# Kernel tuning notes

Hardware: AMD Instinct MI355X
Metric: run time of the kernel (lower is better)

## Reference

```python
import jax, jax.numpy as jnp
import numpy as np


def setup_inputs() -> dict:
    key = jax.random.key(0)
    k1, k2 = jax.random.split(key)
    d, T, n = 256, 8192, 64
    # scale down so exp(ht^T D^T D hj) stays in range, as typical trained D would
    H = jax.random.normal(k1, (d, T), dtype=jnp.float32) * 0.1
    D = jax.random.normal(k2, (n, d), dtype=jnp.float32) * 0.1
    l2 = jnp.ones((), dtype=jnp.float32)
    return {"H": H, "D": D, "l2": l2}


def reference(H, D, l2):
    # H: [d, T], D: [n, d]
    DH = D @ H                                   # [n, T] = D @ H_T.T
    # S[t, j] = h_t^T (D^T D) h_j  == (DH)^T (DH)
    S = jnp.einsum('nt,nj->tj', DH, DH)          # [T, T]
    # beta_j = exp(-0.5 * ||D h_j||^2); row t: attn[t,:] = beta * exp(S[t,:]) / sum
    log_beta = -0.5 * jnp.sum(DH * DH, axis=0)   # [T]
    attn_map = jax.nn.softmax(S + log_beta[None, :], axis=1)  # [T, T]
    Z = l2 * (H @ attn_map)                      # [d, T]
    return Z
```

## Files before the change

kernel.cpp:

```cpp
#include <hip/hip_runtime.h>

#define T_DIM 8192
#define D_DIM 256
#define N_DIM 64
#define LOG2E 1.44269504f

typedef __bf16 bf16x8 __attribute__((ext_vector_type(8)));
typedef __bf16 bf16x4 __attribute__((ext_vector_type(4)));
typedef float f32x16 __attribute__((ext_vector_type(16)));

__device__ __forceinline__ f32x16 zero16() {
  f32x16 v;
#pragma unroll
  for (int i = 0; i < 16; ++i) v[i] = 0.f;
  return v;
}


__global__ __launch_bounds__(256) void k_dh(const float* __restrict__ H,
                                            const float* __restrict__ Dm,
                                            __bf16* __restrict__ DHf,
                                            float* __restrict__ lbe,
                                            float* __restrict__ rowsum) {
  __shared__ __bf16 HlThi[64 * 264];
  __shared__ __bf16 HlTlo[64 * 264];
  __shared__ __bf16 DHs[64 * 72];
  const int tid = threadIdx.x;
  const int t0 = blockIdx.x * 64;
  const int lane = tid & 63;
  const int wave = tid >> 6;
  const int h = lane >> 5;
  const int l31 = lane & 31;
  const float4* H4 = (const float4*)H;
#pragma unroll
  for (int r = 0; r < 16; ++r) {
    int idx = r * 256 + tid;
    int d = idx >> 4, tc = idx & 15;
    float4 v = H4[(size_t)d * (T_DIM / 4) + (t0 >> 2) + tc];
    float vv[4] = {v.x, v.y, v.z, v.w};
#pragma unroll
    for (int i = 0; i < 4; ++i) {
      __bf16 hi = (__bf16)vv[i];
      float lo = vv[i] - (float)hi;
      HlThi[(tc * 4 + i) * 264 + d] = hi;
      HlTlo[(tc * 4 + i) * 264 + d] = (__bf16)lo;
    }
  }
  __syncthreads();
  const int tt = wave & 1, nh = wave >> 1;
  const int m = tt * 32 + l31;
  const int n = nh * 32 + l31;
  f32x16 c = zero16();
  for (int kk = 0; kk < 16; ++kk) {
    bf16x8 ahi = *(const bf16x8*)&HlThi[m * 264 + kk * 16 + h * 8];
    bf16x8 alo = *(const bf16x8*)&HlTlo[m * 264 + kk * 16 + h * 8];
    const float4* dp = (const float4*)(Dm + (size_t)n * 256 + kk * 16 + h * 8);
    float4 b0 = dp[0], b1 = dp[1];
    float bv[8] = {b0.x, b0.y, b0.z, b0.w, b1.x, b1.y, b1.z, b1.w};
    bf16x8 bhi, blo;
#pragma unroll
    for (int i = 0; i < 8; ++i) {
      __bf16 hi = (__bf16)bv[i];
      bhi[i] = hi;
      blo[i] = (__bf16)(bv[i] - (float)hi);
    }
    c = __builtin_amdgcn_mfma_f32_32x32x16_bf16(ahi, bhi, c, 0, 0, 0);
    c = __builtin_amdgcn_mfma_f32_32x32x16_bf16(ahi, blo, c, 0, 0, 0);
    c = __builtin_amdgcn_mfma_f32_32x32x16_bf16(alo, bhi, c, 0, 0, 0);
  }
#pragma unroll
  for (int r = 0; r < 16; ++r) {
    int row = tt * 32 + (r & 3) + 8 * (r >> 2) + 4 * h;
    DHs[row * 72 + n] = (__bf16)c[r];
  }
  __syncthreads();
#pragma unroll
  for (int r = 0; r < 2; ++r) {
    int idx = r * 256 + tid;
    int g = idx >> 8, cc = (idx >> 5) & 7, l = idx & 31;
    bf16x8 w = *(const bf16x8*)&DHs[(g * 32 + l) * 72 + cc * 8];
    *(bf16x8*)(DHf + (size_t)(blockIdx.x * 2 + g) * 2048 + cc * 256 + l * 8) = w;
  }
  if (tid < 64) {
    float s = 0.f;
#pragma unroll
    for (int q = 0; q < 8; ++q) {
      bf16x8 w = *(const bf16x8*)&DHs[tid * 72 + q * 8];
#pragma unroll
      for (int i = 0; i < 8; ++i) { float f = (float)w[i]; s += f * f; }
    }
    lbe[t0 + tid] = -0.5f * s * LOG2E;
    rowsum[t0 + tid] = 0.f;
  }
}

__global__ __launch_bounds__(256, 2) void k_rowsum(const __bf16* __restrict__ DHf,
                                                   const float* __restrict__ lbe,
                                                   float* __restrict__ rowsum) {
  __shared__ float red2[64 * 65];
  const int tid = threadIdx.x;
  const int lane = tid & 63;
  const int wave = tid >> 6;
  const int h = lane >> 5;
  const int tt = wave & 1, jt = wave >> 1;
  const int t0 = (int)(blockIdx.x >> 4) * 64;
  const int jbase = (int)(blockIdx.x & 15) * 512;
  const int Gt = (t0 >> 5) + tt;
  bf16x8 aR[4];
#pragma unroll
  for (int kk = 0; kk < 4; ++kk)
    aR[kk] = *(const bf16x8*)(DHf + (size_t)Gt * 2048 + kk * 512 + lane * 8);
  float racc[16];
#pragma unroll
  for (int r = 0; r < 16; ++r) racc[r] = 0.f;
  for (int jit = 0; jit < 8; ++jit) {
    const size_t Gj = (jbase >> 5) + jit * 2 + jt;
    bf16x8 b[4];
#pragma unroll
    for (int kk = 0; kk < 4; ++kk)
      b[kk] = *(const bf16x8*)(DHf + Gj * 2048 + kk * 512 + lane * 8);
    const float lbv = lbe[jbase + jit * 64 + jt * 32 + (lane & 31)];
    f32x16 s = zero16();
#pragma unroll
    for (int kk = 0; kk < 4; ++kk)
      s = __builtin_amdgcn_mfma_f32_32x32x16_bf16(aR[kk], b[kk], s, 0, 0, 0);
#pragma unroll
    for (int r = 0; r < 16; ++r)
      racc[r] += __builtin_amdgcn_exp2f(__builtin_fmaf(s[r], LOG2E, lbv));
  }
#pragma unroll
  for (int r = 0; r < 16; ++r) {
    int tl = tt * 32 + (r & 3) + 8 * (r >> 2) + 4 * h;
    red2[tl * 65 + jt * 32 + (lane & 31)] = racc[r];
  }
  __syncthreads();
  if (tid < 64) {
    float s = 0.f;
#pragma unroll 8
    for (int c = 0; c < 64; ++c) s += red2[tid * 65 + c];
    atomicAdd(&rowsum[t0 + tid], s);
  }
}

__global__ __launch_bounds__(256) void k_scaleH(const float* __restrict__ H,
                                                const float* __restrict__ rowsum,
                                                __bf16* __restrict__ Hbf_sw,
                                                float* __restrict__ Z) {
  __shared__ float rinvL[64];
  const int tid = threadIdx.x;
  const int bx = blockIdx.x;
  const int tblk = bx >> 1, dh = bx & 1;
  const int t0 = tblk * 64;
  if (tid < 64) rinvL[tid] = 1.0f / rowsum[t0 + tid];
  __syncthreads();
#pragma unroll
  for (int itr = 0; itr < 4; ++itr) {
    int idx = itr * 256 + tid;
    int dl = idx >> 3, tbp = idx & 7;
    int d = dh * 128 + dl;
    int swz = (d ^ (d >> 3)) & 7;
    int tloc = (tbp ^ swz) << 3;
    const float4* hp = (const float4*)(H + (size_t)d * T_DIM + t0 + tloc);
    float4 v0 = hp[0], v1 = hp[1];
    float4 r0 = *(const float4*)&rinvL[tloc];
    float4 r1 = *(const float4*)&rinvL[tloc + 4];
    bf16x8 w;
    w[0] = (__bf16)(v0.x * r0.x); w[1] = (__bf16)(v0.y * r0.y);
    w[2] = (__bf16)(v0.z * r0.z); w[3] = (__bf16)(v0.w * r0.w);
    w[4] = (__bf16)(v1.x * r1.x); w[5] = (__bf16)(v1.y * r1.y);
    w[6] = (__bf16)(v1.z * r1.z); w[7] = (__bf16)(v1.w * r1.w);
    *(bf16x8*)(Hbf_sw + (size_t)tblk * 16384 + (size_t)d * 64 + tbp * 8) = w;
  }
  float4* Z4 = (float4*)Z;
  const int base = bx * 256 + tid;
  const float4 z4 = {0.f, 0.f, 0.f, 0.f};
#pragma unroll
  for (int r = 0; r < 8; ++r) Z4[r * 65536 + base] = z4;
}

__global__ __launch_bounds__(256, 2) void k_z(const __bf16* __restrict__ Hbf_sw,
                                              const __bf16* __restrict__ DHf,
                                              const float* __restrict__ lbe,
                                              const float* __restrict__ l2p,
                                              float* __restrict__ Z) {
  __shared__ __bf16 Hs[256 * 64];
  __shared__ __bf16 Pt[128 * 64];
  const int tid = threadIdx.x;
  const int lane = tid & 63;
  const int wave = tid >> 6;
  const int h = lane >> 5;
  const int l31 = lane & 31;
  const int bx = blockIdx.x;
  const int ts = bx & 7;
  const int j0 = (bx >> 3) * 128;
  const int tbase = ts * 1024;
  const float l2v = l2p[0];
  const int s_tt = wave & 1, s_jg = wave >> 1;
  bf16x8 bS[2][4];
  float lbv[2];
#pragma unroll
  for (int q = 0; q < 2; ++q) {
    const size_t Gj = (j0 >> 5) + s_jg * 2 + q;
#pragma unroll
    for (int kk = 0; kk < 4; ++kk)
      bS[q][kk] = *(const bf16x8*)(DHf + Gj * 2048 + kk * 512 + lane * 8);
    lbv[q] = lbe[j0 + (s_jg * 2 + q) * 32 + l31];
  }
  f32x16 acc[4][2];
#pragma unroll
  for (int u = 0; u < 4; ++u)
#pragma unroll
    for (int v = 0; v < 2; ++v) acc[u][v] = zero16();
  bf16x8 aR[4];
  {
    const size_t Gt = ts * 32 + s_tt;
#pragma unroll
    for (int kk = 0; kk < 4; ++kk)
      aR[kk] = *(const bf16x8*)(DHf + Gt * 2048 + kk * 512 + lane * 8);
  }
  for (int it = 0; it < 16; ++it) {
    const __bf16* gsrc = Hbf_sw + (size_t)(ts * 16 + it) * 16384;
#pragma unroll
    for (int r = 0; r < 8; ++r) {
      int chunk = wave * 8 + r;
      __builtin_amdgcn_global_load_lds(
          (const __attribute__((address_space(1))) unsigned int*)(gsrc + chunk * 512 + lane * 8),
          (__attribute__((address_space(3))) unsigned int*)(Hs + chunk * 512),
          16, 0, 0);
    }
#pragma unroll
    for (int q = 0; q < 2; ++q) {
      f32x16 s = zero16();
#pragma unroll
      for (int kk = 0; kk < 4; ++kk)
        s = __builtin_amdgcn_mfma_f32_32x32x16_bf16(aR[kk], bS[q][kk], s, 0, 0, 0);
      const int jl = (s_jg * 2 + q) * 32 + l31;
      const int sj = (jl ^ (jl >> 3)) & 7;
#pragma unroll
      for (int g = 0; g < 4; ++g) {
        const int tl = s_tt * 32 + g * 8 + 4 * h;
        bf16x4 pv;
        pv[0] = (__bf16)__builtin_amdgcn_exp2f(__builtin_fmaf(s[g * 4 + 0], LOG2E, lbv[q]));
        pv[1] = (__bf16)__builtin_amdgcn_exp2f(__builtin_fmaf(s[g * 4 + 1], LOG2E, lbv[q]));
        pv[2] = (__bf16)__builtin_amdgcn_exp2f(__builtin_fmaf(s[g * 4 + 2], LOG2E, lbv[q]));
        pv[3] = (__bf16)__builtin_amdgcn_exp2f(__builtin_fmaf(s[g * 4 + 3], LOG2E, lbv[q]));
        const int cchunk = tl >> 3;
        *(bf16x4*)&Pt[jl * 64 + ((cchunk ^ sj) << 3) + 4 * h] = pv;
      }
    }
    __syncthreads();
#pragma unroll
    for (int kk = 0; kk < 4; ++kk) {
      const int c = kk * 2 + h;
      bf16x8 af[4], bw[2];
#pragma unroll
      for (int u = 0; u < 4; ++u) {
        int dl = (wave & 1) * 128 + u * 32 + l31;
        af[u] = *(const bf16x8*)&Hs[dl * 64 + ((c ^ ((dl ^ (dl >> 3)) & 7)) << 3)];
      }
#pragma unroll
      for (int v = 0; v < 2; ++v) {
        int j = (wave >> 1) * 64 + v * 32 + l31;
        bw[v] = *(const bf16x8*)&Pt[j * 64 + ((c ^ ((j ^ (j >> 3)) & 7)) << 3)];
      }
#pragma unroll
      for (int u = 0; u < 4; ++u)
#pragma unroll
        for (int v = 0; v < 2; ++v)
          acc[u][v] = __builtin_amdgcn_mfma_f32_32x32x16_bf16(af[u], bw[v], acc[u][v], 0, 0, 0);
    }
    if (it < 15) {
      const size_t Gt = ts * 32 + (it + 1) * 2 + s_tt;
#pragma unroll
      for (int kk = 0; kk < 4; ++kk)
        aR[kk] = *(const bf16x8*)(DHf + Gt * 2048 + kk * 512 + lane * 8);
    }
    __syncthreads();
  }
#pragma unroll
  for (int u = 0; u < 4; ++u)
#pragma unroll
    for (int v = 0; v < 2; ++v)
#pragma unroll
      for (int r = 0; r < 16; ++r) {
        int d = (wave & 1) * 128 + u * 32 + (r & 3) + 8 * (r >> 2) + 4 * h;
        int j = j0 + (wave >> 1) * 64 + v * 32 + l31;
        atomicAdd(&Z[(size_t)d * T_DIM + j], acc[u][v][r] * l2v);
      }
}

extern "C" void kernel_launch(void* const* d_in, const int* in_sizes, int n_in,
                              void* d_out, int out_size, void* d_ws,
                              size_t ws_size, hipStream_t stream) {
  (void)in_sizes; (void)n_in; (void)out_size; (void)ws_size;
  const float* H = (const float*)d_in[0];
  const float* Dm = (const float*)d_in[1];
  const float* l2 = (const float*)d_in[2];
  float* Z = (float*)d_out;
  char* ws = (char*)d_ws;
  __bf16* DHf = (__bf16*)ws;
  float* lbe = (float*)(ws + 1048576);
  float* rowsum = (float*)(ws + 1048576 + 32768);
  __bf16* Hbf_sw = (__bf16*)(ws + 1048576 + 65536);

  k_dh<<<128, 256, 0, stream>>>(H, Dm, DHf, lbe, rowsum);
  k_rowsum<<<2048, 256, 0, stream>>>(DHf, lbe, rowsum);
  k_scaleH<<<256, 256, 0, stream>>>(H, rowsum, Hbf_sw, Z);
  k_z<<<512, 256, 0, stream>>>(Hbf_sw, DHf, lbe, l2, Z);
}
```

Measured before the change: 174.6 us.

## Split d across blocks, double-buffer P, read H fragments directly from global

Restructures the Z kernel so each block handles half of d over a longer t range. H is read straight from global memory in an MFMA-fragment layout written by the scale kernel, replacing the LDS staging. The softmax P tile is double-buffered so computing the next S/exp tile overlaps the current PV matmul with one barrier per iteration. Register use drops to raise occupancy, at the cost of recomputing S/exp in both d-halves and more global traffic for H.

```diff
diff --git a/kernel.cpp b/kernel.cpp
--- a/kernel.cpp
+++ b/kernel.cpp
@@ -144,7 +144,7 @@
 
 __global__ __launch_bounds__(256) void k_scaleH(const float* __restrict__ H,
                                                 const float* __restrict__ rowsum,
-                                                __bf16* __restrict__ Hbf_sw,
+                                                __bf16* __restrict__ Hf,
                                                 float* __restrict__ Z) {
   __shared__ float rinvL[64];
   const int tid = threadIdx.x;
@@ -156,10 +156,9 @@
 #pragma unroll
   for (int itr = 0; itr < 4; ++itr) {
     int idx = itr * 256 + tid;
-    int dl = idx >> 3, tbp = idx & 7;
+    int dl = idx >> 3, c = idx & 7;
     int d = dh * 128 + dl;
-    int swz = (d ^ (d >> 3)) & 7;
-    int tloc = (tbp ^ swz) << 3;
+    int tloc = c * 8;
     const float4* hp = (const float4*)(H + (size_t)d * T_DIM + t0 + tloc);
     float4 v0 = hp[0], v1 = hp[1];
     float4 r0 = *(const float4*)&rinvL[tloc];
@@ -169,7 +168,7 @@
     w[2] = (__bf16)(v0.z * r0.z); w[3] = (__bf16)(v0.w * r0.w);
     w[4] = (__bf16)(v1.x * r1.x); w[5] = (__bf16)(v1.y * r1.y);
     w[6] = (__bf16)(v1.z * r1.z); w[7] = (__bf16)(v1.w * r1.w);
-    *(bf16x8*)(Hbf_sw + (size_t)tblk * 16384 + (size_t)d * 64 + tbp * 8) = w;
+    *(bf16x8*)(Hf + (size_t)(tblk * 8 + (d >> 5)) * 2048 + c * 256 + (d & 31) * 8) = w;
   }
   float4* Z4 = (float4*)Z;
   const int base = bx * 256 + tid;
@@ -178,22 +177,22 @@
   for (int r = 0; r < 8; ++r) Z4[r * 65536 + base] = z4;
 }
 
-__global__ __launch_bounds__(256, 2) void k_z(const __bf16* __restrict__ Hbf_sw,
+__global__ __launch_bounds__(256, 3) void k_z(const __bf16* __restrict__ Hf,
                                               const __bf16* __restrict__ DHf,
                                               const float* __restrict__ lbe,
                                               const float* __restrict__ l2p,
                                               float* __restrict__ Z) {
-  __shared__ __bf16 Hs[256 * 64];
-  __shared__ __bf16 Pt[128 * 64];
+  __shared__ __bf16 Pt[2][128 * 64];
   const int tid = threadIdx.x;
   const int lane = tid & 63;
   const int wave = tid >> 6;
   const int h = lane >> 5;
   const int l31 = lane & 31;
   const int bx = blockIdx.x;
-  const int ts = bx & 7;
+  const int ts = bx & 3;
+  const int dh = (bx >> 2) & 1;
   const int j0 = (bx >> 3) * 128;
-  const int tbase = ts * 1024;
+  const int tbase = ts * 2048;
   const float l2v = l2p[0];
   const int s_tt = wave & 1, s_jg = wave >> 1;
   bf16x8 bS[2][4];
@@ -206,84 +205,88 @@
       bS[q][kk] = *(const bf16x8*)(DHf + Gj * 2048 + kk * 512 + lane * 8);
     lbv[q] = lbe[j0 + (s_jg * 2 + q) * 32 + l31];
   }
-  f32x16 acc[4][2];
-#pragma unroll
-  for (int u = 0; u < 4; ++u)
+  f32x16 acc[2][2];
+#pragma unroll
+  for (int u = 0; u < 2; ++u)
 #pragma unroll
     for (int v = 0; v < 2; ++v) acc[u][v] = zero16();
+
   bf16x8 aR[4];
-  {
-    const size_t Gt = ts * 32 + s_tt;
-#pragma unroll
-    for (int kk = 0; kk < 4; ++kk)
-      aR[kk] = *(const bf16x8*)(DHf + Gt * 2048 + kk * 512 + lane * 8);
-  }
-  for (int it = 0; it < 16; ++it) {
-    const __bf16* gsrc = Hbf_sw + (size_t)(ts * 16 + it) * 16384;
-#pragma unroll
-    for (int r = 0; r < 8; ++r) {
-      int chunk = wave * 8 + r;
-      __builtin_amdgcn_global_load_lds(
-          (const __attribute__((address_space(1))) unsigned int*)(gsrc + chunk * 512 + lane * 8),
-          (__attribute__((address_space(3))) unsigned int*)(Hs + chunk * 512),
-          16, 0, 0);
-    }
-#pragma unroll
-    for (int q = 0; q < 2; ++q) {
-      f32x16 s = zero16();
+#pragma unroll
+  for (int kk = 0; kk < 4; ++kk)
+    aR[kk] = *(const bf16x8*)(DHf + (size_t)(ts * 64 + s_tt) * 2048 + kk * 512 + lane * 8);
+
+#define S_PHASE(p_, it_)                                                        \
+  {                                                                             \
+    _Pragma("unroll") for (int q = 0; q < 2; ++q) {                             \
+      f32x16 s = zero16();                                                      \
+      _Pragma("unroll") for (int kk = 0; kk < 4; ++kk)                          \
+          s = __builtin_amdgcn_mfma_f32_32x32x16_bf16(aR[kk], bS[q][kk], s, 0,  \
+                                                      0, 0);                    \
+      const int jl = (s_jg * 2 + q) * 32 + l31;                                 \
+      const int sj = (jl ^ (jl >> 3)) & 7;                                      \
+      _Pragma("unroll") for (int g = 0; g < 4; ++g) {                           \
+        const int tl = s_tt * 32 + g * 8 + 4 * h;                               \
+        bf16x4 pv;                                                              \
+        pv[0] = (__bf16)__builtin_amdgcn_exp2f(                                 \
+            __builtin_fmaf(s[g * 4 + 0], LOG2E, lbv[q]));                       \
+        pv[1] = (__bf16)__builtin_amdgcn_exp2f(                                 \
+            __builtin_fmaf(s[g * 4 + 1], LOG2E, lbv[q]));                       \
+        pv[2] = (__bf16)__builtin_amdgcn_exp2f(                                 \
+            __builtin_fmaf(s[g * 4 + 2], LOG2E, lbv[q]));                       \
+        pv[3] = (__bf16)__builtin_amdgcn_exp2f(                                 \
+            __builtin_fmaf(s[g * 4 + 3], LOG2E, lbv[q]));                       \
+        const int cchunk = tl >> 3;                                             \
+        *(bf16x4*)&Pt[p_][jl * 64 + ((cchunk ^ sj) << 3) + 4 * h] = pv;         \
+      }                                                                         \
+    }                                                                           \
+  }
+
+  S_PHASE(0, 0);
+#pragma unroll
+  for (int kk = 0; kk < 4; ++kk)
+    aR[kk] = *(const bf16x8*)(DHf + (size_t)(ts * 64 + 2 + s_tt) * 2048 + kk * 512 + lane * 8);
+
+  for (int it = 0; it < 32; ++it) {
+    const int p = it & 1;
+    __syncthreads();
+    if (it < 31) S_PHASE(p ^ 1, it + 1);
+    if (it < 30) {
+      const size_t Gt = ts * 64 + (it + 2) * 2 + s_tt;
 #pragma unroll
       for (int kk = 0; kk < 4; ++kk)
-        s = __builtin_amdgcn_mfma_f32_32x32x16_bf16(aR[kk], bS[q][kk], s, 0, 0, 0);
-      const int jl = (s_jg * 2 + q) * 32 + l31;
-      const int sj = (jl ^ (jl >> 3)) & 7;
-#pragma unroll
-      for (int g = 0; g < 4; ++g) {
-        const int tl = s_tt * 32 + g * 8 + 4 * h;
-        bf16x4 pv;
-        pv[0] = (__bf16)__builtin_amdgcn_exp2f(__builtin_fmaf(s[g * 4 + 0], LOG2E, lbv[q]));
-        pv[1] = (__bf16)__builtin_amdgcn_exp2f(__builtin_fmaf(s[g * 4 + 1], LOG2E, lbv[q]));
-        pv[2] = (__bf16)__builtin_amdgcn_exp2f(__builtin_fmaf(s[g * 4 + 2], LOG2E, lbv[q]));
-        pv[3] = (__bf16)__builtin_amdgcn_exp2f(__builtin_fmaf(s[g * 4 + 3], LOG2E, lbv[q]));
-        const int cchunk = tl >> 3;
-        *(bf16x4*)&Pt[jl * 64 + ((cchunk ^ sj) << 3) + 4 * h] = pv;
+        aR[kk] = *(const bf16x8*)(DHf + Gt * 2048 + kk * 512 + lane * 8);
+    }
+    const size_t hbase = (size_t)((ts * 32 + it) * 8) * 2048;
+#pragma unroll
+    for (int kk = 0; kk < 4; ++kk) {
+      bf16x8 af[2], bw[2];
+#pragma unroll
+      for (int u = 0; u < 2; ++u) {
+        const int dgrp = dh * 4 + (wave & 1) * 2 + u;
+        af[u] = *(const bf16x8*)(Hf + hbase + (size_t)dgrp * 2048 + kk * 512 + lane * 8);
       }
-    }
-    __syncthreads();
-#pragma unroll
-    for (int kk = 0; kk < 4; ++kk) {
       const int c = kk * 2 + h;
-      bf16x8 af[4], bw[2];
-#pragma unroll
-      for (int u = 0; u < 4; ++u) {
-        int dl = (wave & 1) * 128 + u * 32 + l31;
-        af[u] = *(const bf16x8*)&Hs[dl * 64 + ((c ^ ((dl ^ (dl >> 3)) & 7)) << 3)];
-      }
 #pragma unroll
       for (int v = 0; v < 2; ++v) {
         int j = (wave >> 1) * 64 + v * 32 + l31;
-        bw[v] = *(const bf16x8*)&Pt[j * 64 + ((c ^ ((j ^ (j >> 3)) & 7)) << 3)];
+        bw[v] = *(const bf16x8*)&Pt[p][j * 64 + ((c ^ ((j ^ (j >> 3)) & 7)) << 3)];
       }
 #pragma unroll
-      for (int u = 0; u < 4; ++u)
+      for (int u = 0; u < 2; ++u)
 #pragma unroll
         for (int v = 0; v < 2; ++v)
           acc[u][v] = __builtin_amdgcn_mfma_f32_32x32x16_bf16(af[u], bw[v], acc[u][v], 0, 0, 0);
     }
-    if (it < 15) {
-      const size_t Gt = ts * 32 + (it + 1) * 2 + s_tt;
-#pragma unroll
-      for (int kk = 0; kk < 4; ++kk)
-        aR[kk] = *(const bf16x8*)(DHf + Gt * 2048 + kk * 512 + lane * 8);
-    }
-    __syncthreads();
-  }
-#pragma unroll
-  for (int u = 0; u < 4; ++u)
+  }
+#undef S_PHASE
+#pragma unroll
+  for (int u = 0; u < 2; ++u)
 #pragma unroll
     for (int v = 0; v < 2; ++v)
 #pragma unroll
       for (int r = 0; r < 16; ++r) {
-        int d = (wave & 1) * 128 + u * 32 + (r & 3) + 8 * (r >> 2) + 4 * h;
+        int d = dh * 128 + (wave & 1) * 64 + u * 32 + (r & 3) + 8 * (r >> 2) + 4 * h;
         int j = j0 + (wave >> 1) * 64 + v * 32 + l31;
         atomicAdd(&Z[(size_t)d * T_DIM + j], acc[u][v][r] * l2v);
       }
@@ -301,10 +304,10 @@
   __bf16* DHf = (__bf16*)ws;
   float* lbe = (float*)(ws + 1048576);
   float* rowsum = (float*)(ws + 1048576 + 32768);
-  __bf16* Hbf_sw = (__bf16*)(ws + 1048576 + 65536);
+  __bf16* Hf = (__bf16*)(ws + 1048576 + 65536);
 
   k_dh<<<128, 256, 0, stream>>>(H, Dm, DHf, lbe, rowsum);
   k_rowsum<<<2048, 256, 0, stream>>>(DHf, lbe, rowsum);
-  k_scaleH<<<256, 256, 0, stream>>>(H, rowsum, Hbf_sw, Z);
-  k_z<<<512, 256, 0, stream>>>(Hbf_sw, DHf, lbe, l2, Z);
-}
+  k_scaleH<<<256, 256, 0, stream>>>(H, rowsum, Hf, Z);
+  k_z<<<512, 256, 0, stream>>>(Hf, DHf, lbe, l2, Z);
+}
```

Measured after the change: 176.1 us. No clear change (+0.8%).
